# Kernel tuning notes

Hardware: AMD Instinct MI355X
Metric: run time of the kernel (lower is better)

The kernel has to match this reference:

```python
import jax, jax.numpy as jnp
import numpy as np

LAG = 168
HORIZON = 24
D = 6            # d_model = 1 feature + 5-dim position embedding
FF = 18          # dim_feedforward
NL = 3           # num encoder layers
B = 8192
EPS = 1e-5


def setup_inputs() -> dict:
    key = jax.random.key(0)
    ks = jax.random.split(key, 16)
    s = 0.1
    return {
        "input": jax.random.normal(ks[0], (B, LAG), dtype=jnp.float32),
        "pos_emb": jax.random.normal(ks[1], (LAG, 5), dtype=jnp.float32) * s,
        "in_proj_w": jax.random.normal(ks[2], (NL, 3 * D, D), dtype=jnp.float32) * s,
        "in_proj_b": jax.random.normal(ks[3], (NL, 3 * D), dtype=jnp.float32) * s,
        "out_w": jax.random.normal(ks[4], (NL, D, D), dtype=jnp.float32) * s,
        "out_b": jax.random.normal(ks[5], (NL, D), dtype=jnp.float32) * s,
        "ln1_g": jnp.ones((NL, D), dtype=jnp.float32),
        "ln1_b": jnp.zeros((NL, D), dtype=jnp.float32),
        "lin1_w": jax.random.normal(ks[6], (NL, FF, D), dtype=jnp.float32) * s,
        "lin1_b": jax.random.normal(ks[7], (NL, FF), dtype=jnp.float32) * s,
        "lin2_w": jax.random.normal(ks[8], (NL, D, FF), dtype=jnp.float32) * s,
        "lin2_b": jax.random.normal(ks[9], (NL, D), dtype=jnp.float32) * s,
        "ln2_g": jnp.ones((NL, D), dtype=jnp.float32),
        "ln2_b": jnp.zeros((NL, D), dtype=jnp.float32),
        "head_w": jax.random.normal(ks[10], (HORIZON, D * LAG), dtype=jnp.float32) * s,
        "head_b": jax.random.normal(ks[11], (HORIZON,), dtype=jnp.float32) * s,
    }


def _layer_norm(x, g, b):
    m = jnp.mean(x, axis=-1, keepdims=True)
    v = jnp.mean((x - m) ** 2, axis=-1, keepdims=True)
    return (x - m) * jax.lax.rsqrt(v + EPS) * g + b


def reference(input, pos_emb, in_proj_w, in_proj_b, out_w, out_b,
              ln1_g, ln1_b, lin1_w, lin1_b, lin2_w, lin2_b,
              ln2_g, ln2_b, head_w, head_b):
    Bsz, L = input.shape
    # embed positions and concat with raw feature -> [B, L, 6]
    x = jnp.concatenate(
        [input[..., None], jnp.broadcast_to(pos_emb[None], (Bsz, L, 5))], axis=2)

    h = x
    scale = 1.0 / jnp.sqrt(jnp.float32(D))
    for i in range(NL):  # post-norm TransformerEncoderLayer (PyTorch default)
        qkv = jnp.einsum("bld,ed->ble", h, in_proj_w[i]) + in_proj_b[i]  # [B,L,18]
        q, k, v = jnp.split(qkv, 3, axis=-1)  # each [B,L,6], single head
        scores = jnp.einsum("bqd,bkd->bqk", q, k) * scale
        attn = jax.nn.softmax(scores, axis=-1)
        o = jnp.einsum("bqk,bkd->bqd", attn, v)
        o = jnp.einsum("bld,ed->ble", o, out_w[i]) + out_b[i]
        h = _layer_norm(h + o, ln1_g[i], ln1_b[i])
        f = jax.nn.relu(jnp.einsum("bld,fd->blf", h, lin1_w[i]) + lin1_b[i])
        f = jnp.einsum("blf,df->bld", f, lin2_w[i]) + lin2_b[i]
        h = _layer_norm(h + f, ln2_g[i], ln2_b[i])

    h = jax.nn.relu(h + x)              # residual from embedded input + relu
    h = h.reshape(Bsz, L * D)           # flatten
    return h @ head_w.T + head_b        # [B, HORIZON]
```

## Files before the change

### kernel.cpp

```cpp
#include <hip/hip_runtime.h>
#include <math.h>

#define LAG 168
#define HOR 24
#define DM 6
#define FFD 18
#define NL 3
#define WPB 2
#define LNEPS 1e-5f

typedef unsigned int u32;
typedef float f32x4 __attribute__((ext_vector_type(4)));
typedef float f32x16 __attribute__((ext_vector_type(16)));
typedef short s16x8 __attribute__((ext_vector_type(8)));
typedef __bf16 bfx2 __attribute__((ext_vector_type(2)));

#define PP    800
#define SLICE 1376

__device__ __forceinline__ u32 pkbf(float a, float b) {
    bfx2 t; t[0] = (__bf16)a; t[1] = (__bf16)b;
    return __builtin_bit_cast(u32, t);
}
__device__ __forceinline__ s16x8 mk8(u32 a, u32 b, u32 c, u32 d) {
    uint4 u; u.x = a; u.y = b; u.z = c; u.w = d;
    return __builtin_bit_cast(s16x8, u);
}
__device__ __forceinline__ float b2f(unsigned short h) {
    u32 u = ((u32)h) << 16; return __builtin_bit_cast(float, u);
}
__device__ __forceinline__ void ln6(const float* r, const float* g, const float* bb, float* outv) {
    float m = (r[0]+r[1]+r[2]+r[3]+r[4]+r[5]) * (1.0f/6.0f);
    float v = 0.f;
#pragma unroll
    for (int d = 0; d < DM; ++d) { float t = r[d]-m; v += t*t; }
    v *= (1.0f/6.0f);
    float rs = __builtin_amdgcn_rsqf(v + LNEPS);
#pragma unroll
    for (int d = 0; d < DM; ++d) outv[d] = (r[d]-m)*rs*g[d] + bb[d];
}

__global__ __launch_bounds__(64*WPB) void tfenc_kernel(
    const float* __restrict__ input, const float* __restrict__ pos_emb,
    const float* __restrict__ ipw, const float* __restrict__ ipb,
    const float* __restrict__ ow,  const float* __restrict__ obp,
    const float* __restrict__ l1g, const float* __restrict__ l1b,
    const float* __restrict__ f1w, const float* __restrict__ f1b,
    const float* __restrict__ f2w, const float* __restrict__ f2b,
    const float* __restrict__ l2g, const float* __restrict__ l2b,
    const float* __restrict__ hw,  const float* __restrict__ hb,
    float* __restrict__ out)
{
    __shared__ __align__(16) float lds[WPB * SLICE];

    const int L   = threadIdx.x & 63;
    const int wid = threadIdx.x >> 6;
    const int b   = blockIdx.x * WPB + wid;

    float*  sl  = lds + wid * SLICE;
    __bf16* slh = (__bf16*)sl;
    u32*    slu = (u32*)sl;

    float hv[3][DM];
#pragma unroll
    for (int i = 0; i < 3; ++i) {
        int r = L + 64*i;
        bool real = (r < LAG);
        hv[i][0] = real ? input[(size_t)b*LAG + r] : 0.f;
#pragma unroll
        for (int j = 0; j < 5; ++j)
            hv[i][1+j] = real ? pos_emb[r*5 + j] : 0.f;
    }

    const float cQ = 0.5889116917845058f;
    const u32 himask = (L & 32) ? 0u : ~0u;
    const int permA = 4*(L & 31);
    const int permB = permA + 128;

#pragma unroll 1
    for (int il = 0; il < NL; ++il) {
        const float* Wip = ipw + il*3*DM*DM;
        const float* bip = ipb + il*3*DM;
        const float* Wo  = ow  + il*DM*DM;
        const float* bo  = obp + il*DM;
        const float* g1  = l1g + il*DM;     const float* c1  = l1b + il*DM;
        const float* W1  = f1w + il*FFD*DM; const float* bb1 = f1b + il*FFD;
        const float* W2  = f2w + il*DM*FFD; const float* bb2 = f2b + il*DM;
        const float* g2  = l2g + il*DM;     const float* c2  = l2b + il*DM;

        u32 qp[3][3], kp[3][3];
#pragma unroll
        for (int i = 0; i < 3; ++i) {
            int r = L + 64*i;
            float qv[6], kv[6], vv[6];
#pragma unroll
            for (int e = 0; e < 18; ++e) {
                float a = bip[e];
#pragma unroll
                for (int d = 0; d < DM; ++d) a += hv[i][d]*Wip[e*DM+d];
                if (e < 6) qv[e] = a*cQ;
                else if (e < 12) kv[e-6] = a;
                else vv[e-12] = a;
            }
            qp[i][0]=pkbf(qv[0],qv[1]); qp[i][1]=pkbf(qv[2],qv[3]); qp[i][2]=pkbf(qv[4],qv[5]);
            kp[i][0]=pkbf(kv[0],kv[1]); kp[i][1]=pkbf(kv[2],kv[3]); kp[i][2]=pkbf(kv[4],kv[5]);
#pragma unroll
            for (int d = 0; d < DM; ++d)
                slh[d*200 + r] = (__bf16)vv[d];
        }
        {
            __bf16 one = (__bf16)1.0f;
            slh[6*200 + L] = one;
            slh[6*200 + 64 + L] = one;
            slh[6*200 + 128 + L] = one;
        }

        s16x8 kf[6];
#pragma unroll
        for (int kt = 0; kt < 6; ++kt) {
            int adr = (kt & 1) ? permB : permA;
            int slo = kt >> 1;
            u32 w0 = ((u32)__builtin_amdgcn_ds_bpermute(adr, (int)kp[slo][0])) & himask;
            u32 w1 = ((u32)__builtin_amdgcn_ds_bpermute(adr, (int)kp[slo][1])) & himask;
            u32 w2 = ((u32)__builtin_amdgcn_ds_bpermute(adr, (int)kp[slo][2])) & himask;
            kf[kt] = mk8(w0, w1, w2, 0u);
        }
        s16x8 vf[6];
        {
            int d = L & 15;
            int vrow = d < 7 ? d : 7;
            const u32* vb = slu + (vrow*100 + (L >> 4)*4);
#pragma unroll
            for (int kc = 0; kc < 6; ++kc)
                vf[kc] = __builtin_bit_cast(s16x8, *(const uint4*)(vb + kc*16));
        }

        const int wrbase = PP + (L & 31)*18 + 2*(L >> 5);
        const int rdbase = PP + (L & 15)*18 + 4*(L >> 4);

#pragma unroll
        for (int qt = 0; qt < 6; ++qt) {
            int adr = (qt & 1) ? permB : permA;
            int slo = qt >> 1;
            u32 u0 = ((u32)__builtin_amdgcn_ds_bpermute(adr, (int)qp[slo][0])) & himask;
            u32 u1 = ((u32)__builtin_amdgcn_ds_bpermute(adr, (int)qp[slo][1])) & himask;
            u32 u2 = ((u32)__builtin_amdgcn_ds_bpermute(adr, (int)qp[slo][2])) & himask;
            s16x8 qf = mk8(u0, u1, u2, 0u);
            f32x4 acc0 = {0.f,0.f,0.f,0.f};
            f32x4 acc1 = {0.f,0.f,0.f,0.f};
#pragma unroll
            for (int kt = 0; kt < 6; ++kt) {
                const f32x16 z = {};
                __builtin_amdgcn_s_setprio(1);
                f32x16 S = __builtin_amdgcn_mfma_f32_32x32x16_bf16(kf[kt], qf, z, 0, 0, 0);
                __builtin_amdgcn_s_setprio(0);
                u32 w[8];
#pragma unroll
                for (int jj = 0; jj < 8; ++jj) {
                    if (kt == 5 && jj >= 2) w[jj] = 0u;
                    else w[jj] = pkbf(__builtin_amdgcn_exp2f(S[2*jj]),
                                      __builtin_amdgcn_exp2f(S[2*jj+1]));
                }
                u32* ppw = slu + wrbase;
                { uint2 t; t.x=w[0]; t.y=w[1]; *(uint2*)(ppw     ) = t; }
                { uint2 t; t.x=w[2]; t.y=w[3]; *(uint2*)(ppw +  4) = t; }
                { uint2 t; t.x=w[4]; t.y=w[5]; *(uint2*)(ppw +  8) = t; }
                { uint2 t; t.x=w[6]; t.y=w[7]; *(uint2*)(ppw + 12) = t; }
                const u32* rr = slu + rdbase;
                uint2 a00 = *(const uint2*)(rr);
                uint2 a01 = *(const uint2*)(rr + 2);
                uint2 a10 = *(const uint2*)(rr + 288);
                uint2 a11 = *(const uint2*)(rr + 290);
                __builtin_amdgcn_s_setprio(1);
                acc0 = __builtin_amdgcn_mfma_f32_16x16x32_bf16(mk8(a00.x,a00.y,a01.x,a01.y), vf[kt], acc0, 0,0,0);
                acc1 = __builtin_amdgcn_mfma_f32_16x16x32_bf16(mk8(a10.x,a10.y,a11.x,a11.y), vf[kt], acc1, 0,0,0);
                __builtin_amdgcn_s_setprio(0);
            }
            int d = L & 15;
            if (d < 7) {
                int qb = 32*qt + 4*(L >> 4);
#pragma unroll
                for (int r2 = 0; r2 < 4; ++r2) {
                    slh[(qb + r2)*8 + d]      = (__bf16)acc0[r2];
                    slh[(qb + 16 + r2)*8 + d] = (__bf16)acc1[r2];
                }
            }
        }

#pragma unroll
        for (int i = 0; i < 3; ++i) {
            int r = L + 64*i;
            s16x8 ov = __builtin_bit_cast(s16x8, *(const uint4*)(slh + r*8));
            float o[7];
#pragma unroll
            for (int d = 0; d < 7; ++d) o[d] = b2f((unsigned short)ov[d]);
            float inv = __builtin_amdgcn_rcpf(o[6]);
            float att[6], rv[6];
#pragma unroll
            for (int d = 0; d < 6; ++d) att[d] = o[d]*inv;
#pragma unroll
            for (int e = 0; e < 6; ++e) {
                float a = bo[e];
#pragma unroll
                for (int d = 0; d < 6; ++d) a += att[d]*Wo[e*6+d];
                rv[e] = hv[i][e] + a;
            }
            ln6(rv, g1, c1, hv[i]);
            float o2[6];
#pragma unroll
            for (int d = 0; d < 6; ++d) o2[d] = bb2[d];
#pragma unroll
            for (int ff = 0; ff < FFD; ++ff) {
                float a = bb1[ff];
#pragma unroll
                for (int d = 0; d < 6; ++d) a += hv[i][d]*W1[ff*6+d];
                a = fmaxf(a, 0.f);
#pragma unroll
                for (int d = 0; d < 6; ++d) o2[d] += a*W2[d*FFD+ff];
            }
#pragma unroll
            for (int d = 0; d < 6; ++d) rv[d] = hv[i][d] + o2[d];
            ln6(rv, g2, c2, hv[i]);
        }
    }

#pragma unroll
    for (int i = 0; i < 3; ++i) {
        int r = L + 64*i;
        bool real = (r < LAG);
        float x0 = real ? input[(size_t)b*LAG + r] : 0.f;
        sl[r*6 + 0] = real ? fmaxf(hv[i][0] + x0, 0.f) : 0.f;
#pragma unroll
        for (int j = 0; j < 5; ++j) {
            float xj = real ? pos_emb[r*5 + j] : 0.f;
            sl[r*6 + 1 + j] = real ? fmaxf(hv[i][1+j] + xj, 0.f) : 0.f;
        }
    }
    {
        int t = L >> 1, half = L & 1;
        float p = 0.f;
        if (L < 48) {
            const float4* wv  = (const float4*)(hw + (size_t)t*1008 + half*504);
            const float4* hv4 = (const float4*)(sl + half*504);
#pragma unroll 6
            for (int k = 0; k < 126; ++k) {
                float4 w = wv[k], hh = hv4[k];
                p += w.x*hh.x + w.y*hh.y + w.z*hh.z + w.w*hh.w;
            }
        }
        p += __shfl_xor(p, 1);
        if (L < 48 && half == 0)
            out[(size_t)b*HOR + t] = p + hb[t];
    }
}

extern "C" void kernel_launch(void* const* d_in, const int* in_sizes, int n_in,
                              void* d_out, int out_size, void* d_ws, size_t ws_size,
                              hipStream_t stream) {
    const float* input   = (const float*)d_in[0];
    const float* pos_emb = (const float*)d_in[1];
    const float* ipw     = (const float*)d_in[2];
    const float* ipb     = (const float*)d_in[3];
    const float* ow      = (const float*)d_in[4];
    const float* ob      = (const float*)d_in[5];
    const float* l1g     = (const float*)d_in[6];
    const float* l1b     = (const float*)d_in[7];
    const float* f1w     = (const float*)d_in[8];
    const float* f1b     = (const float*)d_in[9];
    const float* f2w     = (const float*)d_in[10];
    const float* f2b     = (const float*)d_in[11];
    const float* l2g     = (const float*)d_in[12];
    const float* l2b     = (const float*)d_in[13];
    const float* hw      = (const float*)d_in[14];
    const float* hb      = (const float*)d_in[15];
    float* out = (float*)d_out;

    const int B = in_sizes[0] / LAG;
    tfenc_kernel<<<dim3(B / WPB), dim3(64 * WPB), 0, stream>>>(
        input, pos_emb, ipw, ipb, ow, ob, l1g, l1b,
        f1w, f1b, f2w, f2b, l2g, l2b, hw, hb, out);
}
```

Baseline: 189.2 us.

## Compute QKV projection with MFMA via LDS staging, one wave per block

Replaces the per-lane scalar QKV projection (18x6 FMAs per row) with a 32x32x16 bf16 MFMA over bf16 hidden states staged in LDS, with the bias folded in through a constant-one column. Q and K fragments are now read directly from LDS instead of being assembled through ds_bpermute shuffles. The launch changes to one 64-thread wave per block with a larger LDS slice, and the s_setprio hints are removed. In exchange it adds bf16 rounding of the hidden state and weights before the projection, plus extra LDS writes every layer.

Result: slower. 236.2 us (+24.8%).

```diff
diff --git a/kernel.cpp b/kernel.cpp
--- a/kernel.cpp
+++ b/kernel.cpp
@@ -6,7 +6,6 @@
 #define DM 6
 #define FFD 18
 #define NL 3
-#define WPB 2
 #define LNEPS 1e-5f
 
 typedef unsigned int u32;
@@ -15,8 +14,15 @@
 typedef short s16x8 __attribute__((ext_vector_type(8)));
 typedef __bf16 bfx2 __attribute__((ext_vector_type(2)));
 
-#define PP    800
-#define SLICE 1376
+#define ZB    0
+#define HB    4
+#define VT    772
+#define QB    1472
+#define KB    2240
+#define PPb   2240
+#define SLICE 3008
+#define HBH   (2*HB)
+#define VTH   (2*VT)
 
 __device__ __forceinline__ u32 pkbf(float a, float b) {
     bfx2 t; t[0] = (__bf16)a; t[1] = (__bf16)b;
@@ -40,7 +46,7 @@
     for (int d = 0; d < DM; ++d) outv[d] = (r[d]-m)*rs*g[d] + bb[d];
 }
 
-__global__ __launch_bounds__(64*WPB) void tfenc_kernel(
+__global__ __launch_bounds__(64) void tfenc_kernel(
     const float* __restrict__ input, const float* __restrict__ pos_emb,
     const float* __restrict__ ipw, const float* __restrict__ ipb,
     const float* __restrict__ ow,  const float* __restrict__ obp,
@@ -51,15 +57,15 @@
     const float* __restrict__ hw,  const float* __restrict__ hb,
     float* __restrict__ out)
 {
-    __shared__ __align__(16) float lds[WPB * SLICE];
-
-    const int L   = threadIdx.x & 63;
-    const int wid = threadIdx.x >> 6;
-    const int b   = blockIdx.x * WPB + wid;
-
-    float*  sl  = lds + wid * SLICE;
+    __shared__ __align__(16) float lds[SLICE];
+    float*  sl  = lds;
     __bf16* slh = (__bf16*)sl;
     u32*    slu = (u32*)sl;
+
+    const int L = threadIdx.x;
+    const int b = blockIdx.x;
+
+    if (L < 4) slu[ZB + L] = 0;
 
     float hv[3][DM];
 #pragma unroll
@@ -71,11 +77,21 @@
         for (int j = 0; j < 5; ++j)
             hv[i][1+j] = real ? pos_emb[r*5 + j] : 0.f;
     }
+#pragma unroll
+    for (int i = 0; i < 3; ++i) {
+        int r = L + 64*i;
+        uint4 hw4;
+        hw4.x = pkbf(hv[i][0], hv[i][1]);
+        hw4.y = pkbf(hv[i][2], hv[i][3]);
+        hw4.z = pkbf(hv[i][4], hv[i][5]);
+        hw4.w = pkbf(1.0f, 0.0f);
+        *(uint4*)(slu + HB + 4*r) = hw4;
+    }
 
     const float cQ = 0.5889116917845058f;
-    const u32 himask = (L & 32) ? 0u : ~0u;
-    const int permA = 4*(L & 31);
-    const int permB = permA + 128;
+    const bool lo = (L < 32);
+    const int  rB = L & 31;
+    const int  tstep = lo ? 128 : 0;
 
 #pragma unroll 1
     for (int il = 0; il < NL; ++il) {
@@ -88,72 +104,82 @@
         const float* W2  = f2w + il*DM*FFD; const float* bb2 = f2b + il*DM;
         const float* g2  = l2g + il*DM;     const float* c2  = l2b + il*DM;
 
-        u32 qp[3][3], kp[3][3];
-#pragma unroll
-        for (int i = 0; i < 3; ++i) {
-            int r = L + 64*i;
-            float qv[6], kv[6], vv[6];
-#pragma unroll
-            for (int e = 0; e < 18; ++e) {
-                float a = bip[e];
-#pragma unroll
-                for (int d = 0; d < DM; ++d) a += hv[i][d]*Wip[e*DM+d];
-                if (e < 6) qv[e] = a*cQ;
-                else if (e < 12) kv[e-6] = a;
-                else vv[e-12] = a;
-            }
-            qp[i][0]=pkbf(qv[0],qv[1]); qp[i][1]=pkbf(qv[2],qv[3]); qp[i][2]=pkbf(qv[4],qv[5]);
-            kp[i][0]=pkbf(kv[0],kv[1]); kp[i][1]=pkbf(kv[2],kv[3]); kp[i][2]=pkbf(kv[4],kv[5]);
-#pragma unroll
-            for (int d = 0; d < DM; ++d)
-                slh[d*200 + r] = (__bf16)vv[d];
+        s16x8 aq;
+        {
+            int m  = rB;
+            int mm = (m < 18) ? m : 0;
+            const float* wrow = Wip + mm*6;
+            float w0 = wrow[0], w1 = wrow[1], w2 = wrow[2];
+            float w3 = wrow[3], w4 = wrow[4], w5 = wrow[5];
+            float bm = bip[mm];
+            float s  = (m < 6) ? cQ : 1.0f;
+            u32 hm = (lo && m < 18) ? ~0u : 0u;
+            aq = mk8(pkbf(w0*s, w1*s) & hm, pkbf(w2*s, w3*s) & hm,
+                     pkbf(w4*s, w5*s) & hm, pkbf(bm*s, 0.f) & hm);
+        }
+
+        const u32* hbp = slu + (lo ? (HB + 4*rB) : ZB);
+#pragma unroll
+        for (int t = 0; t < 6; ++t) {
+            s16x8 hbf = __builtin_bit_cast(s16x8, *(const uint4*)(hbp + tstep*t));
+            const f32x16 z = {};
+            f32x16 c = __builtin_amdgcn_mfma_f32_32x32x16_bf16(aq, hbf, z, 0, 0, 0);
+            int r = rB + 32*t;
+            if (lo) {
+                uint2 qw; qw.x = pkbf(c[0], c[1]); qw.y = pkbf(c[2], c[3]);
+                *(uint2*)(slu + QB + 4*r) = qw;
+                slu[KB + 4*r + 1] = pkbf(c[4], c[5]);
+                slu[KB + 4*r + 2] = pkbf(c[6], c[7]);
+                slh[VTH + 4*200 + r] = (__bf16)c[8];
+                slh[VTH + 5*200 + r] = (__bf16)c[9];
+            } else {
+                uint2 qw; qw.x = pkbf(c[0], c[1]); qw.y = 0u;
+                *(uint2*)(slu + QB + 4*r + 2) = qw;
+                slu[KB + 4*r + 0] = pkbf(c[2], c[3]);
+                slu[KB + 4*r + 3] = 0u;
+                slh[VTH + 0*200 + r] = (__bf16)c[4];
+                slh[VTH + 1*200 + r] = (__bf16)c[5];
+                slh[VTH + 2*200 + r] = (__bf16)c[6];
+                slh[VTH + 3*200 + r] = (__bf16)c[7];
+            }
         }
         {
             __bf16 one = (__bf16)1.0f;
-            slh[6*200 + L] = one;
-            slh[6*200 + 64 + L] = one;
-            slh[6*200 + 128 + L] = one;
+            slh[VTH + 6*200 + L]       = one;
+            slh[VTH + 6*200 + 64 + L]  = one;
+            slh[VTH + 6*200 + 128 + L] = one;
         }
 
         s16x8 kf[6];
-#pragma unroll
-        for (int kt = 0; kt < 6; ++kt) {
-            int adr = (kt & 1) ? permB : permA;
-            int slo = kt >> 1;
-            u32 w0 = ((u32)__builtin_amdgcn_ds_bpermute(adr, (int)kp[slo][0])) & himask;
-            u32 w1 = ((u32)__builtin_amdgcn_ds_bpermute(adr, (int)kp[slo][1])) & himask;
-            u32 w2 = ((u32)__builtin_amdgcn_ds_bpermute(adr, (int)kp[slo][2])) & himask;
-            kf[kt] = mk8(w0, w1, w2, 0u);
+        {
+            const u32* kbp = slu + (lo ? (KB + 4*rB) : ZB);
+#pragma unroll
+            for (int kt = 0; kt < 6; ++kt)
+                kf[kt] = __builtin_bit_cast(s16x8, *(const uint4*)(kbp + tstep*kt));
         }
         s16x8 vf[6];
         {
             int d = L & 15;
-            int vrow = d < 7 ? d : 7;
-            const u32* vb = slu + (vrow*100 + (L >> 4)*4);
+            int vrow = d < 7 ? d : 6;
+            const u32* vb = slu + (VT + vrow*100 + (L >> 4)*4);
 #pragma unroll
             for (int kc = 0; kc < 6; ++kc)
                 vf[kc] = __builtin_bit_cast(s16x8, *(const uint4*)(vb + kc*16));
         }
 
-        const int wrbase = PP + (L & 31)*18 + 2*(L >> 5);
-        const int rdbase = PP + (L & 15)*18 + 4*(L >> 4);
+        const int wrbase = PPb + (L & 31)*18 + 2*(L >> 5);
+        const int rdbase = PPb + (L & 15)*18 + 4*(L >> 4);
+        const u32* qbp = slu + (lo ? (QB + 4*rB) : ZB);
 
 #pragma unroll
         for (int qt = 0; qt < 6; ++qt) {
-            int adr = (qt & 1) ? permB : permA;
-            int slo = qt >> 1;
-            u32 u0 = ((u32)__builtin_amdgcn_ds_bpermute(adr, (int)qp[slo][0])) & himask;
-            u32 u1 = ((u32)__builtin_amdgcn_ds_bpermute(adr, (int)qp[slo][1])) & himask;
-            u32 u2 = ((u32)__builtin_amdgcn_ds_bpermute(adr, (int)qp[slo][2])) & himask;
-            s16x8 qf = mk8(u0, u1, u2, 0u);
+            s16x8 qf = __builtin_bit_cast(s16x8, *(const uint4*)(qbp + tstep*qt));
             f32x4 acc0 = {0.f,0.f,0.f,0.f};
             f32x4 acc1 = {0.f,0.f,0.f,0.f};
 #pragma unroll
             for (int kt = 0; kt < 6; ++kt) {
                 const f32x16 z = {};
-                __builtin_amdgcn_s_setprio(1);
                 f32x16 S = __builtin_amdgcn_mfma_f32_32x32x16_bf16(kf[kt], qf, z, 0, 0, 0);
-                __builtin_amdgcn_s_setprio(0);
                 u32 w[8];
 #pragma unroll
                 for (int jj = 0; jj < 8; ++jj) {
@@ -162,27 +188,25 @@
                                       __builtin_amdgcn_exp2f(S[2*jj+1]));
                 }
                 u32* ppw = slu + wrbase;
-                { uint2 t; t.x=w[0]; t.y=w[1]; *(uint2*)(ppw     ) = t; }
-                { uint2 t; t.x=w[2]; t.y=w[3]; *(uint2*)(ppw +  4) = t; }
-                { uint2 t; t.x=w[4]; t.y=w[5]; *(uint2*)(ppw +  8) = t; }
-                { uint2 t; t.x=w[6]; t.y=w[7]; *(uint2*)(ppw + 12) = t; }
+                { uint2 t2; t2.x=w[0]; t2.y=w[1]; *(uint2*)(ppw     ) = t2; }
+                { uint2 t2; t2.x=w[2]; t2.y=w[3]; *(uint2*)(ppw +  4) = t2; }
+                { uint2 t2; t2.x=w[4]; t2.y=w[5]; *(uint2*)(ppw +  8) = t2; }
+                { uint2 t2; t2.x=w[6]; t2.y=w[7]; *(uint2*)(ppw + 12) = t2; }
                 const u32* rr = slu + rdbase;
                 uint2 a00 = *(const uint2*)(rr);
                 uint2 a01 = *(const uint2*)(rr + 2);
                 uint2 a10 = *(const uint2*)(rr + 288);
                 uint2 a11 = *(const uint2*)(rr + 290);
-                __builtin_amdgcn_s_setprio(1);
                 acc0 = __builtin_amdgcn_mfma_f32_16x16x32_bf16(mk8(a00.x,a00.y,a01.x,a01.y), vf[kt], acc0, 0,0,0);
                 acc1 = __builtin_amdgcn_mfma_f32_16x16x32_bf16(mk8(a10.x,a10.y,a11.x,a11.y), vf[kt], acc1, 0,0,0);
-                __builtin_amdgcn_s_setprio(0);
             }
             int d = L & 15;
             if (d < 7) {
                 int qb = 32*qt + 4*(L >> 4);
 #pragma unroll
                 for (int r2 = 0; r2 < 4; ++r2) {
-                    slh[(qb + r2)*8 + d]      = (__bf16)acc0[r2];
-                    slh[(qb + 16 + r2)*8 + d] = (__bf16)acc1[r2];
+                    slh[HBH + (qb + r2)*8 + d]      = (__bf16)acc0[r2];
+                    slh[HBH + (qb + 16 + r2)*8 + d] = (__bf16)acc1[r2];
                 }
             }
         }
@@ -190,7 +214,7 @@
 #pragma unroll
         for (int i = 0; i < 3; ++i) {
             int r = L + 64*i;
-            s16x8 ov = __builtin_bit_cast(s16x8, *(const uint4*)(slh + r*8));
+            s16x8 ov = __builtin_bit_cast(s16x8, *(const uint4*)(slh + HBH + r*8));
             float o[7];
 #pragma unroll
             for (int d = 0; d < 7; ++d) o[d] = b2f((unsigned short)ov[d]);
@@ -221,6 +245,14 @@
 #pragma unroll
             for (int d = 0; d < 6; ++d) rv[d] = hv[i][d] + o2[d];
             ln6(rv, g2, c2, hv[i]);
+            if (il < 2) {
+                uint4 hw4;
+                hw4.x = pkbf(hv[i][0], hv[i][1]);
+                hw4.y = pkbf(hv[i][2], hv[i][3]);
+                hw4.z = pkbf(hv[i][4], hv[i][5]);
+                hw4.w = pkbf(1.0f, 0.0f);
+                *(uint4*)(slu + HB + 4*r) = hw4;
+            }
         }
     }
 
@@ -276,7 +308,7 @@
     float* out = (float*)d_out;
 
     const int B = in_sizes[0] / LAG;
-    tfenc_kernel<<<dim3(B / WPB), dim3(64 * WPB), 0, stream>>>(
+    tfenc_kernel<<<dim3(B), dim3(64), 0, stream>>>(
         input, pos_emb, ipw, ipb, ow, ob, l1g, l1b,
         f1w, f1b, f2w, f2b, l2g, l2b, hw, hb, out);
 }
```
